# Performance work log

Hardware: AMD Instinct MI355X
Metric: run time of the kernel (lower is better)

The kernel has to match this reference:

```python
import jax, jax.numpy as jnp
import numpy as np

N_HID, N_HEAD, N_K, N_V = 1024, 16, 64, 64
B, S = 2, 2048


def setup_inputs() -> dict:
    key = jax.random.key(0)
    ks = jax.random.split(key, 5)
    w_scale = 1.0 / np.sqrt(N_HID)  # keep pre-softmax logits in a sane range
    x = jax.random.normal(ks[0], (B, S, N_HID), dtype=jnp.float32)
    mask = jax.random.randint(ks[1], (B, S, N_HEAD, S), 0, 2) > 0  # [B, Sq, H, Sk] bool
    W_qkv = jax.random.normal(ks[2], (N_HID, N_HEAD * (2 * N_K + N_V)), dtype=jnp.float32) * w_scale
    b_qkv = jnp.zeros((N_HEAD * (2 * N_K + N_V),), dtype=jnp.float32)
    W_out = jax.random.normal(ks[3], (N_HEAD * N_V, N_HID), dtype=jnp.float32) * w_scale
    b_out = jnp.zeros((N_HID,), dtype=jnp.float32)
    return {"x": x, "mask": mask, "W_qkv": W_qkv, "b_qkv": b_qkv, "W_out": W_out, "b_out": b_out}


def reference(x, mask, W_qkv, b_qkv, W_out, b_out):
    nb, sl, nh = x.shape
    qkv = x @ W_qkv + b_qkv                                  # [B, S, H*(2k+v)]
    qkv = qkv.reshape(nb, sl, N_HEAD, 2 * N_K + N_V).transpose(0, 2, 1, 3)  # [B, H, S, 2k+v]
    q, k, v = qkv[..., :N_K], qkv[..., N_K:2 * N_K], qkv[..., 2 * N_K:]
    qk = jnp.einsum('bhqd,bhkd->bhqk', q, k) / np.sqrt(N_K)  # [B, H, Sq, Sk]
    # original masks on the [B, Sq, H, Sk] view; swap mask axes instead of qk
    mask_bhqk = jnp.swapaxes(mask, 1, 2)                     # [B, H, Sq, Sk]
    qk = jnp.where(mask_bhqk, qk, -jnp.inf)
    attn = jax.nn.softmax(qk, axis=-1)
    ctx = jnp.einsum('bhqk,bhkd->bhqd', attn, v)             # [B, H, S, n_v]
    ctx = ctx.transpose(0, 2, 1, 3).reshape(nb, sl, N_HEAD * N_V)
    out = ctx @ W_out + b_out
    return x + out
```

## Files before the change

### kernel.cpp

```cpp
#include <hip/hip_runtime.h>

#define SEQ 2048
#define NHEAD 16
#define NHID 1024

typedef __attribute__((ext_vector_type(8))) short bf16x8;
typedef __attribute__((ext_vector_type(4))) float f32x4;
typedef unsigned short u16;

__device__ inline u16 f2bf(float f) {
    union { float f; unsigned u; } v; v.f = f;
    unsigned r = v.u + 0x7FFFu + ((v.u >> 16) & 1u);
    return (u16)(r >> 16);
}

typedef __attribute__((address_space(3))) unsigned int  lds_uint;
typedef const __attribute__((address_space(1))) unsigned int glob_uint;
__device__ __forceinline__ void gl2lds16(const void* g, void* l) {
    __builtin_amdgcn_global_load_lds((glob_uint*)(unsigned long long)g,
                                     (lds_uint*)(unsigned int)(unsigned long long)l,
                                     16, 0, 0);
}

__global__ void cast_kernel(const float* __restrict__ in, u16* __restrict__ out, int n4) {
    int i = blockIdx.x * 256 + threadIdx.x;
    if (i < n4) {
        float4 v = ((const float4*)in)[i];
        ushort4 o;
        o.x = f2bf(v.x); o.y = f2bf(v.y); o.z = f2bf(v.z); o.w = f2bf(v.w);
        ((ushort4*)out)[i] = o;
    }
}

__global__ void transpose_cast(const float* __restrict__ in, u16* __restrict__ out, int R, int C) {
    __shared__ float tile[32][33];
    int bx = blockIdx.x * 32, by = blockIdx.y * 32;
    int tx = threadIdx.x & 31, ty = threadIdx.x >> 5;
#pragma unroll
    for (int i = ty; i < 32; i += 8) tile[i][tx] = in[(size_t)(by + i) * C + bx + tx];
    __syncthreads();
#pragma unroll
    for (int i = ty; i < 32; i += 8) out[(size_t)(bx + i) * R + by + tx] = f2bf(tile[tx][i]);
}

__global__ void transpose_v(const u16* __restrict__ in, u16* __restrict__ out) {
    __shared__ u16 tile[32][33];
    int s0 = blockIdx.x * 32, d0 = blockIdx.y * 32, bh = blockIdx.z;
    int tx = threadIdx.x & 31, ty = threadIdx.x >> 5;
    const u16* ip = in + (size_t)bh * SEQ * 64;
    u16* op = out + (size_t)bh * 64 * SEQ;
#pragma unroll
    for (int i = ty; i < 32; i += 8) tile[i][tx] = ip[(size_t)(s0 + i) * 64 + d0 + tx];
    __syncthreads();
#pragma unroll
    for (int i = ty; i < 32; i += 8) op[(size_t)(d0 + i) * SEQ + s0 + tx] = tile[tx][i];
}

__launch_bounds__(256, 2)
__global__ void gemm_qkv(const u16* __restrict__ A, const u16* __restrict__ Bt,
                         const float* __restrict__ bias,
                         u16* __restrict__ qs, u16* __restrict__ ks, u16* __restrict__ vs) {
    __shared__ __align__(16) u16 Alds[128 * 64];
    __shared__ __align__(16) u16 Blds[128 * 64];
    const int tid = threadIdx.x;
    const int m0 = blockIdx.y * 128, n0 = blockIdx.x * 128;
    const int lane = tid & 63, wid = tid >> 6;
    const int wm = (wid & 1) * 64, wn = (wid >> 1) * 64;
    const int col = lane & 15, quad = lane >> 4;
    const int sr = tid >> 3, scg = (tid & 7) * 8;
    f32x4 acc[4][4] = {};
    for (int k0 = 0; k0 < 1024; k0 += 64) {
#pragma unroll
        for (int p = 0; p < 4; p++) {
            int r = sr + p * 32;
            gl2lds16(&A[(size_t)(m0 + r) * 1024 + k0 + scg], &Alds[(p * 32 + wid * 8) * 64]);
            gl2lds16(&Bt[(size_t)(n0 + r) * 1024 + k0 + scg], &Blds[(p * 32 + wid * 8) * 64]);
        }
        __syncthreads();
#pragma unroll
        for (int kc = 0; kc < 2; kc++) {
            bf16x8 af[4], bfr[4];
#pragma unroll
            for (int t = 0; t < 4; t++) {
                af[t]  = *(const bf16x8*)&Alds[(wm + t * 16 + col) * 64 + kc * 32 + quad * 8];
                bfr[t] = *(const bf16x8*)&Blds[(wn + t * 16 + col) * 64 + kc * 32 + quad * 8];
            }
#pragma unroll
            for (int mt = 0; mt < 4; mt++)
#pragma unroll
                for (int nt = 0; nt < 4; nt++)
                    acc[mt][nt] = __builtin_amdgcn_mfma_f32_16x16x32_bf16(af[mt], bfr[nt], acc[mt][nt], 0, 0, 0);
        }
        __syncthreads();
    }
#pragma unroll
    for (int mt = 0; mt < 4; mt++)
#pragma unroll
        for (int nt = 0; nt < 4; nt++)
#pragma unroll
            for (int r = 0; r < 4; r++) {
                int gm = m0 + wm + mt * 16 + quad * 4 + r;
                int gn = n0 + wn + nt * 16 + col;
                float val = acc[mt][nt][r] + bias[gn];
                int b = gm >> 11, s = gm & 2047;
                int h = gn / 192, rr = gn - h * 192;
                size_t base = ((size_t)(b * NHEAD + h) * SEQ + s) * 64;
                if (rr < 64)       qs[base + rr] = f2bf(val * 0.125f);
                else if (rr < 128) ks[base + rr - 64] = f2bf(val);
                else               vs[base + rr - 128] = f2bf(val);
            }
}

#define MFIX 10.0f
__launch_bounds__(256, 3)
__global__ void attn_kernel(const u16* __restrict__ qs, const u16* __restrict__ ks,
                            const u16* __restrict__ vt, const int* __restrict__ mask,
                            u16* __restrict__ ctx) {
    __shared__ __align__(16) u16 Klds[2][64 * 64];
    __shared__ __align__(16) u16 Vlds[2][64 * 64];
    __shared__ __align__(16) u16 Plds[4][16 * 72];
    const int tid = threadIdx.x;
    const int lane = tid & 63, wid = tid >> 6;
    const int col = lane & 15, quad = lane >> 4;
    const int bh = blockIdx.y, b = bh >> 4, h = bh & 15;
    const int q0 = blockIdx.x * 64 + wid * 16;
    const size_t hbase = (size_t)bh * SEQ * 64;

    const int srow = lane >> 3, scol8 = (lane & 7) * 8;

    const u16* qp = qs + hbase + (size_t)(q0 + col) * 64 + quad * 8;
    bf16x8 aq0 = *(const bf16x8*)qp;
    bf16x8 aq1 = *(const bf16x8*)(qp + 32);

    const int* mp[4];
#pragma unroll
    for (int r = 0; r < 4; r++)
        mp[r] = mask + (((size_t)b * SEQ + (q0 + quad * 4 + r)) * NHEAD + h) * SEQ + col;

    float l_i[4] = {0.f, 0.f, 0.f, 0.f};
    f32x4 O[4] = {};

#pragma unroll
    for (int p = 0; p < 2; p++) {
        int rw = wid * 16 + p * 8;
        gl2lds16(&ks[hbase + (size_t)(rw + srow) * 64 + scol8], &Klds[0][rw * 64]);
        gl2lds16(&vt[((size_t)bh * 64 + rw + srow) * SEQ + scol8], &Vlds[0][rw * 64]);
    }
    int mv[4][4];
#pragma unroll
    for (int nt = 0; nt < 4; nt++)
#pragma unroll
        for (int r = 0; r < 4; r++) mv[nt][r] = mp[r][nt * 16];

    for (int it = 0; it < 32; it++) {
        const int cur = it & 1;
        const int kb = it * 64;
        __syncthreads();
        int mvn[4][4];
        if (it < 31) {
#pragma unroll
            for (int p = 0; p < 2; p++) {
                int rw = wid * 16 + p * 8;
                gl2lds16(&ks[hbase + (size_t)(kb + 64 + rw + srow) * 64 + scol8], &Klds[cur ^ 1][rw * 64]);
                gl2lds16(&vt[((size_t)bh * 64 + rw + srow) * SEQ + kb + 64 + scol8], &Vlds[cur ^ 1][rw * 64]);
            }
#pragma unroll
            for (int nt = 0; nt < 4; nt++)
#pragma unroll
                for (int r = 0; r < 4; r++) mvn[nt][r] = mp[r][kb + 64 + nt * 16];
        }

        f32x4 sacc[4];
#pragma unroll
        for (int nt = 0; nt < 4; nt++) {
            bf16x8 b0 = *(const bf16x8*)&Klds[cur][(nt * 16 + col) * 64 + quad * 8];
            bf16x8 b1 = *(const bf16x8*)&Klds[cur][(nt * 16 + col) * 64 + 32 + quad * 8];
            f32x4 z = {};
            z = __builtin_amdgcn_mfma_f32_16x16x32_bf16(aq0, b0, z, 0, 0, 0);
            z = __builtin_amdgcn_mfma_f32_16x16x32_bf16(aq1, b1, z, 0, 0, 0);
            sacc[nt] = z;
        }
#pragma unroll
        for (int nt = 0; nt < 4; nt++)
#pragma unroll
            for (int r = 0; r < 4; r++) {
                float p = mv[nt][r] ? __expf(sacc[nt][r] - MFIX) : 0.f;
                l_i[r] += p;
                Plds[wid][(quad * 4 + r) * 72 + nt * 16 + col] = f2bf(p);
            }
#pragma unroll
        for (int nt = 0; nt < 4; nt++)
#pragma unroll
            for (int r = 0; r < 4; r++) mv[nt][r] = mvn[nt][r];

        bf16x8 ap0 = *(const bf16x8*)&Plds[wid][col * 72 + quad * 8];
        bf16x8 ap1 = *(const bf16x8*)&Plds[wid][col * 72 + 32 + quad * 8];
#pragma unroll
        for (int dt = 0; dt < 4; dt++) {
            bf16x8 bv0 = *(const bf16x8*)&Vlds[cur][(dt * 16 + col) * 64 + quad * 8];
            bf16x8 bv1 = *(const bf16x8*)&Vlds[cur][(dt * 16 + col) * 64 + 32 + quad * 8];
            O[dt] = __builtin_amdgcn_mfma_f32_16x16x32_bf16(ap0, bv0, O[dt], 0, 0, 0);
            O[dt] = __builtin_amdgcn_mfma_f32_16x16x32_bf16(ap1, bv1, O[dt], 0, 0, 0);
        }
    }
    float rinv[4];
#pragma unroll
    for (int r = 0; r < 4; r++) {
        float rs = l_i[r];
        rs += __shfl_xor(rs, 1);
        rs += __shfl_xor(rs, 2);
        rs += __shfl_xor(rs, 4);
        rs += __shfl_xor(rs, 8);
        rinv[r] = 1.f / rs;
    }
#pragma unroll
    for (int dt = 0; dt < 4; dt++)
#pragma unroll
        for (int r = 0; r < 4; r++) {
            float val = O[dt][r] * rinv[r];
            int q = q0 + quad * 4 + r;
            ctx[(size_t)(b * SEQ + q) * NHID + h * 64 + dt * 16 + col] = f2bf(val);
        }
}

__launch_bounds__(256, 2)
__global__ void gemm_out(const u16* __restrict__ A, const u16* __restrict__ Bt,
                         const float* __restrict__ bias, const float* __restrict__ xres,
                         float* __restrict__ out) {
    __shared__ __align__(16) u16 Alds[128 * 64];
    __shared__ __align__(16) u16 Blds[128 * 64];
    const int tid = threadIdx.x;
    const int m0 = blockIdx.y * 128, n0 = blockIdx.x * 128;
    const int lane = tid & 63, wid = tid >> 6;
    const int wm = (wid & 1) * 64, wn = (wid >> 1) * 64;
    const int col = lane & 15, quad = lane >> 4;
    const int sr = tid >> 3, scg = (tid & 7) * 8;
    f32x4 acc[4][4] = {};
    for (int k0 = 0; k0 < 1024; k0 += 64) {
#pragma unroll
        for (int p = 0; p < 4; p++) {
            int r = sr + p * 32;
            gl2lds16(&A[(size_t)(m0 + r) * 1024 + k0 + scg], &Alds[(p * 32 + wid * 8) * 64]);
            gl2lds16(&Bt[(size_t)(n0 + r) * 1024 + k0 + scg], &Blds[(p * 32 + wid * 8) * 64]);
        }
        __syncthreads();
#pragma unroll
        for (int kc = 0; kc < 2; kc++) {
            bf16x8 af[4], bfr[4];
#pragma unroll
            for (int t = 0; t < 4; t++) {
                af[t]  = *(const bf16x8*)&Alds[(wm + t * 16 + col) * 64 + kc * 32 + quad * 8];
                bfr[t] = *(const bf16x8*)&Blds[(wn + t * 16 + col) * 64 + kc * 32 + quad * 8];
            }
#pragma unroll
            for (int mt = 0; mt < 4; mt++)
#pragma unroll
                for (int nt = 0; nt < 4; nt++)
                    acc[mt][nt] = __builtin_amdgcn_mfma_f32_16x16x32_bf16(af[mt], bfr[nt], acc[mt][nt], 0, 0, 0);
        }
        __syncthreads();
    }
#pragma unroll
    for (int mt = 0; mt < 4; mt++)
#pragma unroll
        for (int nt = 0; nt < 4; nt++)
#pragma unroll
            for (int r = 0; r < 4; r++) {
                int gm = m0 + wm + mt * 16 + quad * 4 + r;
                int gn = n0 + wn + nt * 16 + col;
                out[(size_t)gm * NHID + gn] = acc[mt][nt][r] + bias[gn] + xres[(size_t)gm * NHID + gn];
            }
}

extern "C" void kernel_launch(void* const* d_in, const int* in_sizes, int n_in,
                              void* d_out, int out_size, void* d_ws, size_t ws_size,
                              hipStream_t stream) {
    const float* x     = (const float*)d_in[0];
    const int*   mask  = (const int*)d_in[1];
    const float* W_qkv = (const float*)d_in[2];
    const float* b_qkv = (const float*)d_in[3];
    const float* W_out = (const float*)d_in[4];
    const float* b_out = (const float*)d_in[5];
    float* out = (float*)d_out;

    char* ws = (char*)d_ws;
    u16* x_bf   = (u16*)(ws);
    u16* wqkv_t = (u16*)(ws + (size_t)(8  << 20));
    u16* wout_t = (u16*)(ws + (size_t)(14 << 20));
    u16* qs     = (u16*)(ws + (size_t)(16 << 20));
    u16* ks     = (u16*)(ws + (size_t)(24 << 20));
    u16* vs     = (u16*)(ws + (size_t)(32 << 20));
    u16* vt     = (u16*)(ws + (size_t)(40 << 20));
    u16* ctx    = (u16*)(ws + (size_t)(48 << 20));

    cast_kernel<<<4096, 256, 0, stream>>>(x, x_bf, 4096 * 1024 / 4);
    transpose_cast<<<dim3(3072 / 32, 1024 / 32), 256, 0, stream>>>(W_qkv, wqkv_t, 1024, 3072);
    transpose_cast<<<dim3(1024 / 32, 1024 / 32), 256, 0, stream>>>(W_out, wout_t, 1024, 1024);
    gemm_qkv<<<dim3(24, 32), 256, 0, stream>>>(x_bf, wqkv_t, b_qkv, qs, ks, vs);
    transpose_v<<<dim3(SEQ / 32, 2, 32), 256, 0, stream>>>(vs, vt);
    attn_kernel<<<dim3(32, 32), 256, 0, stream>>>(qs, ks, vt, mask, ctx);
    gemm_out<<<dim3(8, 32), 256, 0, stream>>>(ctx, wout_t, b_out, x, out);
}
```

Baseline: 830.0 us.

## Transpose attention MFMA operands so each lane owns a query row

Swaps the A/B operands of both attention MFMAs, so the accumulator holds S^T and O^T and each lane owns one query row with four consecutive keys. Mask reads become one int4 vector load per tile instead of scalar loads. P stores to LDS, the final ctx writes become 4-wide vectors, and the row-sum reduction shrinks to two shuffles. The mask prefetch one tile ahead is dropped, so mask load latency is now exposed inside the loop.

```diff
diff --git a/kernel.cpp b/kernel.cpp
--- a/kernel.cpp
+++ b/kernel.cpp
@@ -118,7 +118,7 @@
                             u16* __restrict__ ctx) {
     __shared__ __align__(16) u16 Klds[2][64 * 64];
     __shared__ __align__(16) u16 Vlds[2][64 * 64];
-    __shared__ __align__(16) u16 Plds[4][16 * 72];
+    __shared__ __align__(16) u16 Pst[4][16 * 72];
     const int tid = threadIdx.x;
     const int lane = tid & 63, wid = tid >> 6;
     const int col = lane & 15, quad = lane >> 4;
@@ -132,12 +132,9 @@
     bf16x8 aq0 = *(const bf16x8*)qp;
     bf16x8 aq1 = *(const bf16x8*)(qp + 32);
 
-    const int* mp[4];
-#pragma unroll
-    for (int r = 0; r < 4; r++)
-        mp[r] = mask + (((size_t)b * SEQ + (q0 + quad * 4 + r)) * NHEAD + h) * SEQ + col;
-
-    float l_i[4] = {0.f, 0.f, 0.f, 0.f};
+    const int* mp = mask + (((size_t)b * SEQ + (q0 + col)) * NHEAD + h) * SEQ + quad * 4;
+
+    float l_lane = 0.f;
     f32x4 O[4] = {};
 
 #pragma unroll
@@ -146,17 +143,11 @@
         gl2lds16(&ks[hbase + (size_t)(rw + srow) * 64 + scol8], &Klds[0][rw * 64]);
         gl2lds16(&vt[((size_t)bh * 64 + rw + srow) * SEQ + scol8], &Vlds[0][rw * 64]);
     }
-    int mv[4][4];
-#pragma unroll
-    for (int nt = 0; nt < 4; nt++)
-#pragma unroll
-        for (int r = 0; r < 4; r++) mv[nt][r] = mp[r][nt * 16];
 
     for (int it = 0; it < 32; it++) {
         const int cur = it & 1;
         const int kb = it * 64;
         __syncthreads();
-        int mvn[4][4];
         if (it < 31) {
 #pragma unroll
             for (int p = 0; p < 2; p++) {
@@ -164,63 +155,57 @@
                 gl2lds16(&ks[hbase + (size_t)(kb + 64 + rw + srow) * 64 + scol8], &Klds[cur ^ 1][rw * 64]);
                 gl2lds16(&vt[((size_t)bh * 64 + rw + srow) * SEQ + kb + 64 + scol8], &Vlds[cur ^ 1][rw * 64]);
             }
-#pragma unroll
-            for (int nt = 0; nt < 4; nt++)
-#pragma unroll
-                for (int r = 0; r < 4; r++) mvn[nt][r] = mp[r][kb + 64 + nt * 16];
-        }
-
-        f32x4 sacc[4];
+        }
+        int4 mv[4];
+#pragma unroll
+        for (int nt = 0; nt < 4; nt++) mv[nt] = *(const int4*)(mp + kb + nt * 16);
+
+        f32x4 st[4];
 #pragma unroll
         for (int nt = 0; nt < 4; nt++) {
-            bf16x8 b0 = *(const bf16x8*)&Klds[cur][(nt * 16 + col) * 64 + quad * 8];
-            bf16x8 b1 = *(const bf16x8*)&Klds[cur][(nt * 16 + col) * 64 + 32 + quad * 8];
+            bf16x8 ka0 = *(const bf16x8*)&Klds[cur][(nt * 16 + col) * 64 + quad * 8];
+            bf16x8 ka1 = *(const bf16x8*)&Klds[cur][(nt * 16 + col) * 64 + 32 + quad * 8];
             f32x4 z = {};
-            z = __builtin_amdgcn_mfma_f32_16x16x32_bf16(aq0, b0, z, 0, 0, 0);
-            z = __builtin_amdgcn_mfma_f32_16x16x32_bf16(aq1, b1, z, 0, 0, 0);
-            sacc[nt] = z;
-        }
-#pragma unroll
-        for (int nt = 0; nt < 4; nt++)
-#pragma unroll
-            for (int r = 0; r < 4; r++) {
-                float p = mv[nt][r] ? __expf(sacc[nt][r] - MFIX) : 0.f;
-                l_i[r] += p;
-                Plds[wid][(quad * 4 + r) * 72 + nt * 16 + col] = f2bf(p);
-            }
-#pragma unroll
-        for (int nt = 0; nt < 4; nt++)
-#pragma unroll
-            for (int r = 0; r < 4; r++) mv[nt][r] = mvn[nt][r];
-
-        bf16x8 ap0 = *(const bf16x8*)&Plds[wid][col * 72 + quad * 8];
-        bf16x8 ap1 = *(const bf16x8*)&Plds[wid][col * 72 + 32 + quad * 8];
+            z = __builtin_amdgcn_mfma_f32_16x16x32_bf16(ka0, aq0, z, 0, 0, 0);
+            z = __builtin_amdgcn_mfma_f32_16x16x32_bf16(ka1, aq1, z, 0, 0, 0);
+            st[nt] = z;
+        }
+#pragma unroll
+        for (int nt = 0; nt < 4; nt++) {
+            const int* mw = &mv[nt].x;
+            float p0 = mw[0] ? __expf(st[nt][0] - MFIX) : 0.f;
+            float p1 = mw[1] ? __expf(st[nt][1] - MFIX) : 0.f;
+            float p2 = mw[2] ? __expf(st[nt][2] - MFIX) : 0.f;
+            float p3 = mw[3] ? __expf(st[nt][3] - MFIX) : 0.f;
+            l_lane += (p0 + p1) + (p2 + p3);
+            ushort4 pw;
+            pw.x = f2bf(p0); pw.y = f2bf(p1); pw.z = f2bf(p2); pw.w = f2bf(p3);
+            *(ushort4*)&Pst[wid][col * 72 + nt * 16 + quad * 4] = pw;
+        }
+
+        bf16x8 bp0 = *(const bf16x8*)&Pst[wid][col * 72 + quad * 8];
+        bf16x8 bp1 = *(const bf16x8*)&Pst[wid][col * 72 + 32 + quad * 8];
 #pragma unroll
         for (int dt = 0; dt < 4; dt++) {
-            bf16x8 bv0 = *(const bf16x8*)&Vlds[cur][(dt * 16 + col) * 64 + quad * 8];
-            bf16x8 bv1 = *(const bf16x8*)&Vlds[cur][(dt * 16 + col) * 64 + 32 + quad * 8];
-            O[dt] = __builtin_amdgcn_mfma_f32_16x16x32_bf16(ap0, bv0, O[dt], 0, 0, 0);
-            O[dt] = __builtin_amdgcn_mfma_f32_16x16x32_bf16(ap1, bv1, O[dt], 0, 0, 0);
-        }
-    }
-    float rinv[4];
-#pragma unroll
-    for (int r = 0; r < 4; r++) {
-        float rs = l_i[r];
-        rs += __shfl_xor(rs, 1);
-        rs += __shfl_xor(rs, 2);
-        rs += __shfl_xor(rs, 4);
-        rs += __shfl_xor(rs, 8);
-        rinv[r] = 1.f / rs;
-    }
-#pragma unroll
-    for (int dt = 0; dt < 4; dt++)
-#pragma unroll
-        for (int r = 0; r < 4; r++) {
-            float val = O[dt][r] * rinv[r];
-            int q = q0 + quad * 4 + r;
-            ctx[(size_t)(b * SEQ + q) * NHID + h * 64 + dt * 16 + col] = f2bf(val);
-        }
+            bf16x8 va0 = *(const bf16x8*)&Vlds[cur][(dt * 16 + col) * 64 + quad * 8];
+            bf16x8 va1 = *(const bf16x8*)&Vlds[cur][(dt * 16 + col) * 64 + 32 + quad * 8];
+            O[dt] = __builtin_amdgcn_mfma_f32_16x16x32_bf16(va0, bp0, O[dt], 0, 0, 0);
+            O[dt] = __builtin_amdgcn_mfma_f32_16x16x32_bf16(va1, bp1, O[dt], 0, 0, 0);
+        }
+    }
+    l_lane += __shfl_xor(l_lane, 16);
+    l_lane += __shfl_xor(l_lane, 32);
+    float rinv = 1.f / l_lane;
+    const int q = q0 + col;
+#pragma unroll
+    for (int dt = 0; dt < 4; dt++) {
+        ushort4 o;
+        o.x = f2bf(O[dt][0] * rinv);
+        o.y = f2bf(O[dt][1] * rinv);
+        o.z = f2bf(O[dt][2] * rinv);
+        o.w = f2bf(O[dt][3] * rinv);
+        *(ushort4*)&ctx[(size_t)(b * SEQ + q) * NHID + h * 64 + dt * 16 + quad * 4] = o;
+    }
 }
 
 __launch_bounds__(256, 2)
```

New measurement: 842.8 us. About the same (+1.6%).
